# Optimization experiments

Measured on AMD Instinct MI355X. Metric: run time of the kernel, lower is better.

The kernel has to match this reference:

```python
import jax, jax.numpy as jnp
import numpy as np

EMBED = 32; HEADS = 4; HD = 8; FFN = 64; OBS = 64; CTX = 128; BATCH = 16
INIT_SCALE = 1.0 / np.sqrt(2.0 * 5.0)  # 1/sqrt(2*(3 spatial + 2 temporal))


def rmsnorm(x, w, eps=1e-6):
    return x / jnp.sqrt(jnp.mean(x * x, axis=-1, keepdims=True) + eps) * w


def rope_cache(T):
    theta = 1.0 / (10000.0 ** (jnp.arange(0, HD, 2, dtype=jnp.float32) / HD))
    freqs = jnp.arange(T, dtype=jnp.float32)[:, None] * theta[None, :]  # [T, HD//2]
    return jnp.cos(freqs), jnp.sin(freqs)


def apply_rope(x, cos, sin):
    half = x.shape[-1] // 2
    x1, x2 = x[..., :half], x[..., half:]
    c, s = cos[None, None], sin[None, None]  # broadcast over [B, H, T, HD//2]
    return jnp.concatenate([x1 * c - x2 * s, x2 * c + x1 * s], axis=-1)


def attn_block(x, Wq, Wk, Wv, Wo, Wg, Wval, Wout, norm4, qkn, cos=None, sin=None):
    B, S, W = x.shape
    h = rmsnorm(x, norm4[0])

    def proj(Wm):
        return jnp.einsum('bsw,dw->bsd', h, Wm).reshape(B, S, HEADS, HD).transpose(0, 2, 1, 3)

    q = rmsnorm(proj(Wq), qkn[0])
    k = rmsnorm(proj(Wk), qkn[1])
    v = proj(Wv)
    if cos is not None:
        q = apply_rope(q, cos, sin)
        k = apply_rope(k, cos, sin)
    scores = jnp.einsum('bhqd,bhkd->bhqk', q, k) / np.float32(np.sqrt(HD))
    o = jnp.einsum('bhqk,bhkd->bhqd', jax.nn.softmax(scores, axis=-1), v)
    o = o.transpose(0, 2, 1, 3).reshape(B, S, W)
    x = x + rmsnorm(jnp.einsum('bsw,dw->bsd', o, Wo), norm4[1])
    h2 = rmsnorm(x, norm4[2])
    ffn = jax.nn.silu(jnp.einsum('bsw,fw->bsf', h2, Wg)) * jnp.einsum('bsw,fw->bsf', h2, Wval)
    x = x + rmsnorm(jnp.einsum('bsf,wf->bsw', ffn, Wout), norm4[3])
    return x


def setup_inputs():
    key = jax.random.key(0)
    ks = iter(jax.random.split(key, 40))
    sd = 1.0 / np.sqrt(EMBED)
    inp = {
        'obs_seq': jax.random.normal(next(ks), (BATCH, CTX, OBS), jnp.float32),
        'W_val': jax.random.normal(next(ks), (EMBED, 1), jnp.float32),
        'b_val': jnp.zeros((EMBED,), jnp.float32),
        'input_norm_w': jnp.ones((EMBED,), jnp.float32),
        'dim_embed': jax.random.normal(next(ks), (OBS, EMBED), jnp.float32),
        'cls_tokens': jax.random.normal(next(ks), (3, EMBED), jnp.float32) * sd,
        'final_norm_w': jnp.ones((EMBED,), jnp.float32),
    }
    for pre, n in (('s', 3), ('t', 2)):
        inp[pre + '_Wq'] = jax.random.normal(next(ks), (n, EMBED, EMBED), jnp.float32) * sd
        inp[pre + '_Wk'] = jax.random.normal(next(ks), (n, EMBED, EMBED), jnp.float32) * sd
        inp[pre + '_Wv'] = jax.random.normal(next(ks), (n, EMBED, EMBED), jnp.float32) * sd
        inp[pre + '_Wo'] = jax.random.normal(next(ks), (n, EMBED, EMBED), jnp.float32) * (0.1 * INIT_SCALE * sd)
        inp[pre + '_Wg'] = jax.random.normal(next(ks), (n, FFN, EMBED), jnp.float32) * sd
        inp[pre + '_Wval'] = jax.random.normal(next(ks), (n, FFN, EMBED), jnp.float32) * sd
        inp[pre + '_Wout'] = jax.random.normal(next(ks), (n, EMBED, FFN), jnp.float32) * (INIT_SCALE / np.sqrt(FFN))
        inp[pre + '_norm4'] = jnp.ones((n, 4, EMBED), jnp.float32)
        inp[pre + '_qkn'] = jnp.ones((n, 2, HD), jnp.float32)
    return inp


def reference(obs_seq, W_val, b_val, input_norm_w, dim_embed, cls_tokens, final_norm_w,
              s_Wq, s_Wk, s_Wv, s_Wo, s_Wg, s_Wval, s_Wout, s_norm4, s_qkn,
              t_Wq, t_Wk, t_Wv, t_Wo, t_Wg, t_Wval, t_Wout, t_norm4, t_qkn):
    B, T, D = obs_seq.shape
    slots = D + 3
    # value_proj: Linear(1, EMBED) applied to each scalar feature
    tok = obs_seq[..., None] * W_val[:, 0] + b_val            # [B, T, D, EMBED]
    tok = tok + dim_embed[None, None]                          # dim id embedding
    cls = jnp.broadcast_to(cls_tokens[None, None], (B, T, 3, EMBED))
    tokens = rmsnorm(jnp.concatenate([tok, cls], axis=2), input_norm_w)  # [B,T,slots,EMBED]
    cos, sin = rope_cache(T)

    def spatial(tk, i):
        x = tk.reshape(B * T, slots, EMBED)
        x = attn_block(x, s_Wq[i], s_Wk[i], s_Wv[i], s_Wo[i], s_Wg[i], s_Wval[i], s_Wout[i], s_norm4[i], s_qkn[i])
        return x.reshape(B, T, slots, EMBED)

    def temporal(tk, i):
        x = tk.transpose(0, 2, 1, 3).reshape(B * slots, T, EMBED)
        x = attn_block(x, t_Wq[i], t_Wk[i], t_Wv[i], t_Wo[i], t_Wg[i], t_Wval[i], t_Wout[i], t_norm4[i], t_qkn[i], cos, sin)
        return x.reshape(B, slots, T, EMBED).transpose(0, 2, 1, 3)

    tokens = spatial(tokens, 0)
    tokens = temporal(tokens, 0)
    tokens = spatial(tokens, 1)
    tokens = temporal(tokens, 1)
    tokens = spatial(tokens, 2)
    tokens = rmsnorm(tokens, final_norm_w)
    last = tokens[:, -1]  # [B, slots, EMBED]
    return last[:, D], last[:, D + 1], last[:, D + 2]
```

## Files before the change

kernel.cpp:

```cpp
#include <hip/hip_runtime.h>

#define B_ 16
#define T_ 128
#define OBS_ 64
#define SLOTS_ 67
#define E_ 32
#define H_ 4
#define HD_ 8
#define FFN_ 64

typedef _Float16 h2 __attribute__((ext_vector_type(2)));
typedef _Float16 h4 __attribute__((ext_vector_type(4)));
typedef _Float16 h8 __attribute__((ext_vector_type(8)));
typedef __fp16 mh4 __attribute__((ext_vector_type(4)));
typedef __fp16 mh8 __attribute__((ext_vector_type(8)));
typedef float fx4 __attribute__((ext_vector_type(4)));
union H4u { h4 v; h2 h[2]; };

#define WBLK 10240
#define X16_BYTES (B_ * T_ * SLOTS_ * E_ * 2)
#define W16_BYTES (5 * WBLK * 2)
#define ROPE_OFF (X16_BYTES + W16_BYTES)
#define EMBED_BLOCKS (B_ * T_ * SLOTS_ / 64)

__device__ __forceinline__ float red32(float v) {
  v += __shfl_xor(v, 16); v += __shfl_xor(v, 8); v += __shfl_xor(v, 4);
  v += __shfl_xor(v, 2);  v += __shfl_xor(v, 1);
  return v;
}
__device__ __forceinline__ float red8(float v) {
  v += __shfl_xor(v, 4); v += __shfl_xor(v, 2); v += __shfl_xor(v, 1);
  return v;
}
__device__ __forceinline__ float bfly16(float v) {
  v += __shfl_xor(v, 1); v += __shfl_xor(v, 2);
  v += __shfl_xor(v, 4); v += __shfl_xor(v, 8);
  return v;
}
__device__ __forceinline__ h2 pkrtz(float x, float y) {
  return __builtin_bit_cast(h2, __builtin_amdgcn_cvt_pkrtz(x, y));
}
__device__ __forceinline__ float rcp_(float x) { return __builtin_amdgcn_rcpf(x); }
__device__ __forceinline__ float rsq_(float x) { return __builtin_amdgcn_rsqf(x); }
__device__ __forceinline__ fx4 mfma16(h8 a, h8 b, fx4 c) {
  return __builtin_amdgcn_mfma_f32_16x16x32_f16(
      __builtin_bit_cast(mh8, a), __builtin_bit_cast(mh8, b), c, 0, 0, 0);
}
__device__ __forceinline__ fx4 mfma16k16(h4 a, h4 b, fx4 c) {
  return __builtin_amdgcn_mfma_f32_16x16x16f16(
      __builtin_bit_cast(mh4, a), __builtin_bit_cast(mh4, b), c, 0, 0, 0);
}

__device__ __forceinline__ int sw32(int row, int col) {
  return row * 32 + (col ^ (((row >> 1) & 3) << 3));
}
__device__ __forceinline__ int sw64(int row, int col) {
  return row * 64 + (col ^ ((row & 7) << 3));
}

struct WPtrs {
  const float *sWq, *sWk, *sWv, *sWo, *sWg, *sWvl, *sWout;
  const float *tWq, *tWk, *tWv, *tWo, *tWg, *tWvl, *tWout;
};

#define CVT_BLOCKS 100

__global__ __launch_bounds__(256) void setup_kernel(
    WPtrs p, _Float16* __restrict__ dst,
    const float* __restrict__ obs, const float* __restrict__ Wval,
    const float* __restrict__ bval, const float* __restrict__ innw,
    const float* __restrict__ dimemb, const float* __restrict__ cls,
    float2* __restrict__ rope, _Float16* __restrict__ X) {
  if (blockIdx.x < CVT_BLOCKS) {
    int i = blockIdx.x * 256 + threadIdx.x;
    const int total_pairs = 5 * WBLK / 2;
    if (i >= total_pairs) return;
    int blk = i / (WBLK / 2);
    int f = (i % (WBLK / 2)) * 2;
    bool sp = blk < 3;
    int bi = sp ? blk : blk - 3;
    const float* src;
    int o;
    if (f < 1024)      { src = (sp ? p.sWq : p.tWq) + bi * 1024;  o = f; }
    else if (f < 2048) { src = (sp ? p.sWk : p.tWk) + bi * 1024;  o = f - 1024; }
    else if (f < 3072) { src = (sp ? p.sWv : p.tWv) + bi * 1024;  o = f - 2048; }
    else if (f < 4096) { src = (sp ? p.sWo : p.tWo) + bi * 1024;  o = f - 3072; }
    else if (f < 6144) { src = (sp ? p.sWg : p.tWg) + bi * 2048;  o = f - 4096; }
    else if (f < 8192) { src = (sp ? p.sWvl : p.tWvl) + bi * 2048; o = f - 6144; }
    else               { src = (sp ? p.sWout : p.tWout) + bi * 2048; o = f - 8192; }
    ((h2*)dst)[i] = pkrtz(src[o], src[o + 1]);
  } else if (blockIdx.x < CVT_BLOCKS + EMBED_BLOCKS) {
    int t0 = (blockIdx.x - CVT_BLOCKS) * 64 + (threadIdx.x >> 5);
    int e = threadIdx.x & 31;
#pragma unroll
    for (int i = 0; i < 8; i++) {
      int tok = t0 + i * 8;
      int slot = tok % SLOTS_;
      int bt = tok / SLOTS_;
      float v;
      if (slot < OBS_) {
        float o = obs[bt * OBS_ + slot];
        v = o * Wval[e] + bval[e] + dimemb[slot * E_ + e];
      } else {
        v = cls[(slot - OBS_) * E_ + e];
      }
      float ss = red32(v * v);
      X[tok * E_ + e] = (_Float16)(v * rsq_(ss * (1.0f / E_) + 1e-6f) * innw[e]);
    }
  } else {
    for (int i = threadIdx.x; i < T_ * 4; i += 256) {
      int pos = i >> 2, j = i & 3;
      float th = __builtin_amdgcn_exp2f(-(float)j * 3.3219280948873623f);
      float sv, cv;
      __sincosf((float)pos * th, &sv, &cv);
      rope[i] = make_float2(cv, sv);
    }
  }
}

template <int SV, int SP, bool TEMPORAL, bool LAST>
__device__ __forceinline__ void block_body(
    _Float16* __restrict__ X, const _Float16* __restrict__ W16,
    const float* __restrict__ norm4, const float* __restrict__ qkn,
    const float2* __restrict__ rope, const float* __restrict__ fnw,
    float* __restrict__ out, int bid) {
  constexpr int MT = SP / 16;
  constexpr int MTW = (MT + 3) / 4;
  constexpr int VSTRIDE = TEMPORAL ? 128 : 168;
  constexpr int VROWS = TEMPORAL ? 32 : 33;
  __shared__ __align__(16) _Float16 smem[SP * 96 + VROWS * VSTRIDE];
  _Float16* hb = smem;
  _Float16* qb = smem + SP * 32;
  _Float16* kb = smem + SP * 64;
  _Float16* vT = smem + SP * 96;
  _Float16* ffnb = qb;

  const int tid = threadIdx.x;
  const int l = tid & 63, wv = tid >> 6;
  const int lm = l & 15, lq = l >> 4, hd = l & 7;

  auto vt_idx = [](int d, int s) {
    if (TEMPORAL) return d * 128 + (((s & ~15) ^ ((d & 7) << 4)) | (s & 15));
    return d * VSTRIDE + s;
  };

  int base, stride;
  if (TEMPORAL) {
    int b = bid / SLOTS_;
    int slot = bid % SLOTS_;
    base = (b * T_ * SLOTS_ + slot) * E_;
    stride = SLOTS_ * E_;
  } else {
    base = bid * 2 * SLOTS_ * E_;
    stride = E_;
  }

  const float nw0a = norm4[lm],      nw0b = norm4[16 + lm];
  const float nw1a = norm4[32 + lm], nw1b = norm4[48 + lm];
  const float nw2a = norm4[64 + lm], nw2b = norm4[80 + lm];
  const float nw3a = norm4[96 + lm], nw3b = norm4[112 + lm];
  const fx4 fz = {0.f, 0.f, 0.f, 0.f};
  const float qw = qkn[hd], kw = qkn[8 + hd];
  const float qscale = 0.35355339059327373f * 1.4426950408889634f;

  float xr[MTW][4][2];
#pragma unroll
  for (int t = 0; t < MTW; t++) {
    int mt = wv + 4 * t;
    if (mt < MT) {
#pragma unroll
      for (int r = 0; r < 4; r++) {
        int s = mt * 16 + lq * 4 + r;
        bool ok = (SV == SP) || (s < SV);
        int off = base + s * stride;
        xr[t][r][0] = ok ? (float)X[off + lm] : 0.f;
        xr[t][r][1] = ok ? (float)X[off + 16 + lm] : 0.f;
      }
    }
  }
#pragma unroll
  for (int t = 0; t < MTW; t++) {
    int mt = wv + 4 * t;
    if (mt < MT) {
#pragma unroll
      for (int r = 0; r < 4; r++) {
        int s = mt * 16 + lq * 4 + r;
        float p = bfly16(xr[t][r][0] * xr[t][r][0] + xr[t][r][1] * xr[t][r][1]);
        float inv = rsq_(p * (1.0f / E_) + 1e-6f);
        if (SV == SP || s < SV) {
          hb[sw32(s, lm)] = (_Float16)(xr[t][r][0] * inv * nw0a);
          hb[sw32(s, 16 + lm)] = (_Float16)(xr[t][r][1] * inv * nw0b);
        }
      }
    }
  }
  __syncthreads();

  for (int u = wv; u < MT * 2; u += 4) {
    const int mt = u >> 1, nt = u & 1;
    h8 aH = *(const h8*)(hb + sw32(mt * 16 + lm, lq * 8));
    float rc[4], rs[4];
    if (TEMPORAL) {
#pragma unroll
      for (int r = 0; r < 4; r++) {
        float2 cs = rope[(mt * 16 + lq * 4 + r) * 4 + (hd & 3)];
        rc[r] = cs.x; rs[r] = cs.y;
      }
    }
    const int d = nt * 16 + lm;
    h8 bq = *(const h8*)(W16 + (nt * 16 + lm) * 32 + lq * 8);
    h8 bk = *(const h8*)(W16 + 1024 + (nt * 16 + lm) * 32 + lq * 8);
    h8 bv = *(const h8*)(W16 + 2048 + (nt * 16 + lm) * 32 + lq * 8);
    fx4 aq = mfma16(aH, bq, fz);
    fx4 ak = mfma16(aH, bk, fz);
    fx4 av = mfma16(aH, bv, fz);
#pragma unroll
    for (int r = 0; r < 4; r++) {
      int s = mt * 16 + lq * 4 + r;
      float q1 = aq[r], k1 = ak[r];
      float qv = q1 * rsq_(red8(q1 * q1) * 0.125f + 1e-6f) * qw;
      float kv = k1 * rsq_(red8(k1 * k1) * 0.125f + 1e-6f) * kw;
      if (TEMPORAL) {
        float qp = __shfl_xor(qv, 4);
        float kp = __shfl_xor(kv, 4);
        qv = (hd < 4) ? (qv * rc[r] - qp * rs[r]) : (qv * rc[r] + qp * rs[r]);
        kv = (hd < 4) ? (kv * rc[r] - kp * rs[r]) : (kv * rc[r] + kp * rs[r]);
      }
      if (SV == SP || s < SV) {
        qb[sw32(s, d)] = (_Float16)(qv * qscale);
        kb[sw32(s, d)] = (_Float16)kv;
      }
    }
    const int s0 = mt * 16 + lq * 4;
    const int va = vt_idx(d, s0);
    if (SV == SP || s0 + 1 < SV) *(h2*)(vT + va) = pkrtz(av[0], av[1]);
    if (SV == SP || s0 + 3 < SV) *(h2*)(vT + va + 2) = pkrtz(av[2], av[3]);
  }
  if (!TEMPORAL) {
    for (int idx = tid; idx < 32 * 13; idx += 256) {
      int d = idx / 13, c = 2 * SLOTS_ + 2 * (idx % 13);
      *(h2*)(vT + d * VSTRIDE + c) = pkrtz(0.f, 0.f);
    }
    for (int idx = tid; idx < VSTRIDE / 2; idx += 256) {
      *(h2*)(vT + 32 * VSTRIDE + 2 * idx) = pkrtz(1.f, 1.f);
    }
  }
  __syncthreads();

  {
    const int h = wv;
    const h8 z8 = {};
    const h4 ones4 = {(_Float16)1.f, (_Float16)1.f, (_Float16)1.f, (_Float16)1.f};
    const bool vlane = (lm < 8);
    const int dv = h * 8 + (lm & 7);
    const int vrow = (!TEMPORAL && !vlane) ? 32 : dv;

    auto loadQ = [&](int mt) {
      h8 b = *(const h8*)(qb + sw32(mt * 16 + lm, lq * 8));
      return (lq == h) ? b : z8;
    };
    auto maskx = [&](float x, int kidx, int mode, int q) {
      if (mode == 1) return (kidx < SLOTS_) ? x : 0.f;
      if (mode == 2) return (kidx >= SLOTS_) ? x : 0.f;
      if (mode == 3) return (kidx < 2 * SLOTS_) ? x : 0.f;
      if (mode == 4) {
        bool ok = (kidx < 2 * SLOTS_) && ((kidx < SLOTS_) == (q < SLOTS_));
        return ok ? x : 0.f;
      }
      return x;
    };
    auto ktile2 = [&](int kt, int mode, const h8& bQ0, const h8& bQ1,
                      fx4& o0, fx4& o1) {
      h8 aK = *(const h8*)(kb + sw32(kt * 16 + lm, lq * 8));
      fx4 s0 = mfma16(aK, bQ0, fz);
      fx4 s1 = mfma16(aK, bQ1, fz);
      float e0[4], e1[4];
#pragma unroll
      for (int r = 0; r < 4; r++) {
        int kidx = kt * 16 + lq * 4 + r;
        e0[r] = maskx(__builtin_amdgcn_exp2f(s0[r]), kidx, mode, 0);
        e1[r] = maskx(__builtin_amdgcn_exp2f(s1[r]), kidx, mode, 0);
      }
      H4u p0, p1;
      p0.h[0] = pkrtz(e0[0], e0[1]); p0.h[1] = pkrtz(e0[2], e0[3]);
      p1.h[0] = pkrtz(e1[0], e1[1]); p1.h[1] = pkrtz(e1[2], e1[3]);
      h4 aV = *(const h4*)(vT + vt_idx(vrow, kt * 16 + lq * 4));
      if (TEMPORAL) aV = vlane ? aV : ones4;
      o0 = mfma16k16(aV, p0.v, o0);
      o1 = mfma16k16(aV, p1.v, o1);
    };
    auto ktile1 = [&](int kt, int mode, int q, const h8& bQ, fx4& oa) {
      h8 aK = *(const h8*)(kb + sw32(kt * 16 + lm, lq * 8));
      fx4 sc = mfma16(aK, bQ, fz);
      float ev[4];
#pragma unroll
      for (int r = 0; r < 4; r++) {
        int kidx = kt * 16 + lq * 4 + r;
        ev[r] = maskx(__builtin_amdgcn_exp2f(sc[r]), kidx, mode, q);
      }
      H4u pT;
      pT.h[0] = pkrtz(ev[0], ev[1]); pT.h[1] = pkrtz(ev[2], ev[3]);
      h4 aV = *(const h4*)(vT + vt_idx(vrow, kt * 16 + lq * 4));
      if (TEMPORAL) aV = vlane ? aV : ones4;
      oa = mfma16k16(aV, pT.v, oa);
    };
    auto finish = [&](int mt, fx4& oa) {
      int q = mt * 16 + lm;
      float lsum = __shfl_xor(oa[0], 32);
      float inv = rcp_(lsum);
      if (lq < 2 && (SV == SP || q < SV)) {
        H4u ov;
        ov.h[0] = pkrtz(oa[0] * inv, oa[1] * inv);
        ov.h[1] = pkrtz(oa[2] * inv, oa[3] * inv);
        *(h4*)(hb + sw32(q, h * 8 + lq * 4)) = ov.v;
      }
    };

    if (TEMPORAL) {
      for (int mtp = 0; mtp < MT / 2; mtp++) {
        h8 bQ0 = loadQ(2 * mtp), bQ1 = loadQ(2 * mtp + 1);
        fx4 o0 = fz, o1 = fz;
#pragma unroll
        for (int kt = 0; kt < MT; kt++) ktile2(kt, 0, bQ0, bQ1, o0, o1);
        finish(2 * mtp, o0);
        finish(2 * mtp + 1, o1);
      }
    } else {
      for (int mtp = 0; mtp < 2; mtp++) {
        h8 bQ0 = loadQ(2 * mtp), bQ1 = loadQ(2 * mtp + 1);
        fx4 o0 = fz, o1 = fz;
#pragma unroll
        for (int kt = 0; kt < 4; kt++) ktile2(kt, 0, bQ0, bQ1, o0, o1);
        ktile2(4, 1, bQ0, bQ1, o0, o1);
        finish(2 * mtp, o0);
        finish(2 * mtp + 1, o1);
      }
      {
        h8 bQ = loadQ(4);
        fx4 oa = fz;
        const int q = 4 * 16 + lm;
#pragma unroll
        for (int kt = 0; kt < MT; kt++) ktile1(kt, 4, q, bQ, oa);
        finish(4, oa);
      }
      for (int mtp = 0; mtp < 2; mtp++) {
        int m0 = 5 + 2 * mtp;
        h8 bQ0 = loadQ(m0), bQ1 = loadQ(m0 + 1);
        fx4 o0 = fz, o1 = fz;
        ktile2(4, 2, bQ0, bQ1, o0, o1);
#pragma unroll
        for (int kt = 5; kt < 8; kt++) ktile2(kt, 0, bQ0, bQ1, o0, o1);
        ktile2(8, 3, bQ0, bQ1, o0, o1);
        finish(m0, o0);
        finish(m0 + 1, o1);
      }
    }
  }
  __syncthreads();

#pragma unroll
  for (int t = 0; t < MTW; t++) {
    int mt = wv + 4 * t;
    if (mt < MT) {
      h8 aO = *(const h8*)(hb + sw32(mt * 16 + lm, lq * 8));
      h8 b0 = *(const h8*)(W16 + 3072 + lm * 32 + lq * 8);
      h8 b1 = *(const h8*)(W16 + 3072 + (16 + lm) * 32 + lq * 8);
      fx4 a0 = mfma16(aO, b0, fz);
      fx4 a1 = mfma16(aO, b1, fz);
#pragma unroll
      for (int r = 0; r < 4; r++) {
        int s = mt * 16 + lq * 4 + r;
        float p = bfly16(a0[r] * a0[r] + a1[r] * a1[r]);
        float inv = rsq_(p * (1.0f / E_) + 1e-6f);
        xr[t][r][0] += a0[r] * inv * nw1a;
        xr[t][r][1] += a1[r] * inv * nw1b;
        float q2 = bfly16(xr[t][r][0] * xr[t][r][0] + xr[t][r][1] * xr[t][r][1]);
        float inv2 = rsq_(q2 * (1.0f / E_) + 1e-6f);
        if (SV == SP || s < SV) {
          hb[sw32(s, lm)] = (_Float16)(xr[t][r][0] * inv2 * nw2a);
          hb[sw32(s, 16 + lm)] = (_Float16)(xr[t][r][1] * inv2 * nw2b);
        }
      }
    }
  }
  __syncthreads();

  for (int u = wv; u < MT * 4; u += 4) {
    const int mt = u >> 2, nt = u & 3;
    h8 aH2 = *(const h8*)(hb + sw32(mt * 16 + lm, lq * 8));
    h8 bg = *(const h8*)(W16 + 4096 + (nt * 16 + lm) * 32 + lq * 8);
    h8 bl = *(const h8*)(W16 + 6144 + (nt * 16 + lm) * 32 + lq * 8);
    fx4 g = mfma16(aH2, bg, fz);
    fx4 vvv = mfma16(aH2, bl, fz);
#pragma unroll
    for (int r = 0; r < 4; r++) {
      int s = mt * 16 + lq * 4 + r;
      if (SV == SP || s < SV) {
        float gg = g[r];
        float sg = gg * rcp_(1.0f + __builtin_amdgcn_exp2f(gg * -1.4426950408889634f));
        ffnb[sw64(s, nt * 16 + lm)] = (_Float16)(sg * vvv[r]);
      }
    }
  }
  __syncthreads();

#pragma unroll
  for (int t = 0; t < MTW; t++) {
    int mt = wv + 4 * t;
    if (mt < MT) {
      const int row = mt * 16 + lm;
      h8 a0 = *(const h8*)(ffnb + sw64(row, lq * 8));
      h8 a1 = *(const h8*)(ffnb + sw64(row, 32 + lq * 8));
      h8 b00 = *(const h8*)(W16 + 8192 + lm * 64 + lq * 8);
      h8 b01 = *(const h8*)(W16 + 8192 + lm * 64 + 32 + lq * 8);
      h8 b10 = *(const h8*)(W16 + 8192 + (16 + lm) * 64 + lq * 8);
      h8 b11 = *(const h8*)(W16 + 8192 + (16 + lm) * 64 + 32 + lq * 8);
      fx4 o0 = mfma16(a1, b01, mfma16(a0, b00, fz));
      fx4 o1 = mfma16(a1, b11, mfma16(a0, b10, fz));
#pragma unroll
      for (int r = 0; r < 4; r++) {
        int s = mt * 16 + lq * 4 + r;
        float p = bfly16(o0[r] * o0[r] + o1[r] * o1[r]);
        float inv = rsq_(p * (1.0f / E_) + 1e-6f);
        xr[t][r][0] += o0[r] * inv * nw3a;
        xr[t][r][1] += o1[r] * inv * nw3b;
        if (SV == SP || s < SV) {
          int off = base + s * stride;
          X[off + lm] = (_Float16)xr[t][r][0];
          X[off + 16 + lm] = (_Float16)xr[t][r][1];
        }
      }
      if (LAST && mt == MT - 1 && (bid & (T_ / 2 - 1)) == (T_ / 2 - 1)) {
        const int b = bid / (T_ / 2);
#pragma unroll
        for (int r = 0; r < 4; r++) {
          int s = mt * 16 + lq * 4 + r;
          int j = s - (SLOTS_ + OBS_);
          float p2 = bfly16(xr[t][r][0] * xr[t][r][0] + xr[t][r][1] * xr[t][r][1]);
          if (j >= 0 && j < 3) {
            float inv2 = rsq_(p2 * (1.0f / E_) + 1e-6f);
            out[j * (B_ * E_) + b * E_ + lm] = xr[t][r][0] * inv2 * fnw[lm];
            out[j * (B_ * E_) + b * E_ + 16 + lm] = xr[t][r][1] * inv2 * fnw[16 + lm];
          }
        }
      }
    }
  }
}

__global__ __launch_bounds__(256, 4) void attn_spatial_kernel(
    _Float16* __restrict__ X, const _Float16* __restrict__ W16,
    const float* __restrict__ norm4, const float* __restrict__ qkn) {
  block_body<2 * SLOTS_, 144, false, false>(X, W16, norm4, qkn, nullptr,
                                            nullptr, nullptr, blockIdx.x);
}

__global__ __launch_bounds__(256, 4) void attn_spatial_last_kernel(
    _Float16* __restrict__ X, const _Float16* __restrict__ W16,
    const float* __restrict__ norm4, const float* __restrict__ qkn,
    const float* __restrict__ fnw, float* __restrict__ out) {
  block_body<2 * SLOTS_, 144, false, true>(X, W16, norm4, qkn, nullptr,
                                           fnw, out, blockIdx.x);
}

__global__ __launch_bounds__(256, 5) void attn_temporal_kernel(
    _Float16* __restrict__ X, const _Float16* __restrict__ W16,
    const float* __restrict__ norm4, const float* __restrict__ qkn,
    const float2* __restrict__ rope) {
  block_body<T_, 128, true, false>(X, W16, norm4, qkn, rope,
                                   nullptr, nullptr, blockIdx.x);
}

extern "C" void kernel_launch(void* const* d_in, const int* in_sizes, int n_in,
                              void* d_out, int out_size, void* d_ws, size_t ws_size,
                              hipStream_t stream) {
  (void)in_sizes; (void)n_in; (void)out_size; (void)ws_size;
  const float* obs          = (const float*)d_in[0];
  const float* W_val        = (const float*)d_in[1];
  const float* b_val        = (const float*)d_in[2];
  const float* input_norm_w = (const float*)d_in[3];
  const float* dim_embed    = (const float*)d_in[4];
  const float* cls_tokens   = (const float*)d_in[5];
  const float* final_norm_w = (const float*)d_in[6];
  const float* s_n4   = (const float*)d_in[14];
  const float* s_qkn  = (const float*)d_in[15];
  const float* t_n4   = (const float*)d_in[23];
  const float* t_qkn  = (const float*)d_in[24];

  _Float16* X = (_Float16*)d_ws;
  _Float16* W16 = (_Float16*)((char*)d_ws + X16_BYTES);
  float2* rope = (float2*)((char*)d_ws + ROPE_OFF);
  float* out = (float*)d_out;

  WPtrs wp;
  wp.sWq   = (const float*)d_in[7];
  wp.sWk   = (const float*)d_in[8];
  wp.sWv   = (const float*)d_in[9];
  wp.sWo   = (const float*)d_in[10];
  wp.sWg   = (const float*)d_in[11];
  wp.sWvl  = (const float*)d_in[12];
  wp.sWout = (const float*)d_in[13];
  wp.tWq   = (const float*)d_in[16];
  wp.tWk   = (const float*)d_in[17];
  wp.tWv   = (const float*)d_in[18];
  wp.tWo   = (const float*)d_in[19];
  wp.tWg   = (const float*)d_in[20];
  wp.tWvl  = (const float*)d_in[21];
  wp.tWout = (const float*)d_in[22];

  setup_kernel<<<CVT_BLOCKS + EMBED_BLOCKS + 1, 256, 0, stream>>>(
      wp, W16, obs, W_val, b_val, input_norm_w, dim_embed, cls_tokens, rope, X);

  const int N4 = 4 * E_;
  const int QN = 2 * HD_;

#define SPATIAL(i)                                                     \
  attn_spatial_kernel<<<B_ * T_ / 2, 256, 0, stream>>>(                \
      X, W16 + (i)*WBLK, s_n4 + (i)*N4, s_qkn + (i)*QN)
#define TEMPORAL(i)                                                    \
  attn_temporal_kernel<<<B_ * SLOTS_, 256, 0, stream>>>(               \
      X, W16 + (3 + (i)) * WBLK, t_n4 + (i)*N4, t_qkn + (i)*QN, rope)

  SPATIAL(0);
  TEMPORAL(0);
  SPATIAL(1);
  TEMPORAL(1);
  attn_spatial_last_kernel<<<B_ * T_ / 2, 256, 0, stream>>>(
      X, W16 + 2 * WBLK, s_n4 + 2 * N4, s_qkn + 2 * QN, final_norm_w, out);

#undef SPATIAL
#undef TEMPORAL
}
```

Before: 312.3 us.

## Hoist weights and K/V/Q fragments into registers, prefetch LDS tiles in projections

Each wave now loads its fixed weight columns once for the QKV, output, gate and down projections, and prefetches the next activation tile from LDS while computing the current one. The attention stage preloads all K, V and Q fragments into register arrays before looping, and the temporal path now processes four query tiles per key pass instead of two. The embed kernel drops to one token per warp with more blocks. These changes cut repeated LDS and global loads and expose more independent MFMA work, at the cost of more register pressure, which may reduce occupancy under launch_bounds(256,4).

```diff
diff --git a/kernel.cpp b/kernel.cpp
--- a/kernel.cpp
+++ b/kernel.cpp
@@ -21,7 +21,7 @@
 #define X16_BYTES (B_ * T_ * SLOTS_ * E_ * 2)
 #define W16_BYTES (5 * WBLK * 2)
 #define ROPE_OFF (X16_BYTES + W16_BYTES)
-#define EMBED_BLOCKS (B_ * T_ * SLOTS_ / 64)
+#define EMBED_BLOCKS ((B_ * T_ * SLOTS_ + 7) / 8)
 
 __device__ __forceinline__ float red32(float v) {
   v += __shfl_xor(v, 16); v += __shfl_xor(v, 8); v += __shfl_xor(v, 4);
@@ -90,23 +90,21 @@
     else               { src = (sp ? p.sWout : p.tWout) + bi * 2048; o = f - 8192; }
     ((h2*)dst)[i] = pkrtz(src[o], src[o + 1]);
   } else if (blockIdx.x < CVT_BLOCKS + EMBED_BLOCKS) {
-    int t0 = (blockIdx.x - CVT_BLOCKS) * 64 + (threadIdx.x >> 5);
+    int tok = (blockIdx.x - CVT_BLOCKS) * 8 + (threadIdx.x >> 5);
     int e = threadIdx.x & 31;
-#pragma unroll
-    for (int i = 0; i < 8; i++) {
-      int tok = t0 + i * 8;
-      int slot = tok % SLOTS_;
-      int bt = tok / SLOTS_;
-      float v;
-      if (slot < OBS_) {
-        float o = obs[bt * OBS_ + slot];
-        v = o * Wval[e] + bval[e] + dimemb[slot * E_ + e];
-      } else {
-        v = cls[(slot - OBS_) * E_ + e];
-      }
-      float ss = red32(v * v);
-      X[tok * E_ + e] = (_Float16)(v * rsq_(ss * (1.0f / E_) + 1e-6f) * innw[e]);
-    }
+    const int total = B_ * T_ * SLOTS_;
+    if (tok >= total) return;
+    int slot = tok % SLOTS_;
+    int bt = tok / SLOTS_;
+    float v;
+    if (slot < OBS_) {
+      float o = obs[bt * OBS_ + slot];
+      v = o * Wval[e] + bval[e] + dimemb[slot * E_ + e];
+    } else {
+      v = cls[(slot - OBS_) * E_ + e];
+    }
+    float ss = red32(v * v);
+    X[tok * E_ + e] = (_Float16)(v * rsq_(ss * (1.0f / E_) + 1e-6f) * innw[e]);
   } else {
     for (int i = threadIdx.x; i < T_ * 4; i += 256) {
       int pos = i >> 2, j = i & 3;
@@ -196,45 +194,53 @@
   }
   __syncthreads();
 
-  for (int u = wv; u < MT * 2; u += 4) {
-    const int mt = u >> 1, nt = u & 1;
-    h8 aH = *(const h8*)(hb + sw32(mt * 16 + lm, lq * 8));
-    float rc[4], rs[4];
-    if (TEMPORAL) {
+  {
+    const int ntw = wv & 1;
+    const int d = ntw * 16 + lm;
+    h8 bqw = *(const h8*)(W16 + (ntw * 16 + lm) * 32 + lq * 8);
+    h8 bkw = *(const h8*)(W16 + 1024 + (ntw * 16 + lm) * 32 + lq * 8);
+    h8 bvw = *(const h8*)(W16 + 2048 + (ntw * 16 + lm) * 32 + lq * 8);
+    int u = wv;
+    h8 aH = *(const h8*)(hb + sw32((u >> 1) * 16 + lm, lq * 8));
+    for (; u < MT * 2; u += 4) {
+      h8 aHn;
+      if (u + 4 < MT * 2)
+        aHn = *(const h8*)(hb + sw32(((u + 4) >> 1) * 16 + lm, lq * 8));
+      const int mt = u >> 1;
+      float rc[4], rs[4];
+      if (TEMPORAL) {
+#pragma unroll
+        for (int r = 0; r < 4; r++) {
+          float2 cs = rope[(mt * 16 + lq * 4 + r) * 4 + (hd & 3)];
+          rc[r] = cs.x; rs[r] = cs.y;
+        }
+      }
+      fx4 aq = mfma16(aH, bqw, fz);
+      fx4 ak = mfma16(aH, bkw, fz);
+      fx4 av = mfma16(aH, bvw, fz);
 #pragma unroll
       for (int r = 0; r < 4; r++) {
-        float2 cs = rope[(mt * 16 + lq * 4 + r) * 4 + (hd & 3)];
-        rc[r] = cs.x; rs[r] = cs.y;
-      }
-    }
-    const int d = nt * 16 + lm;
-    h8 bq = *(const h8*)(W16 + (nt * 16 + lm) * 32 + lq * 8);
-    h8 bk = *(const h8*)(W16 + 1024 + (nt * 16 + lm) * 32 + lq * 8);
-    h8 bv = *(const h8*)(W16 + 2048 + (nt * 16 + lm) * 32 + lq * 8);
-    fx4 aq = mfma16(aH, bq, fz);
-    fx4 ak = mfma16(aH, bk, fz);
-    fx4 av = mfma16(aH, bv, fz);
-#pragma unroll
-    for (int r = 0; r < 4; r++) {
-      int s = mt * 16 + lq * 4 + r;
-      float q1 = aq[r], k1 = ak[r];
-      float qv = q1 * rsq_(red8(q1 * q1) * 0.125f + 1e-6f) * qw;
-      float kv = k1 * rsq_(red8(k1 * k1) * 0.125f + 1e-6f) * kw;
-      if (TEMPORAL) {
-        float qp = __shfl_xor(qv, 4);
-        float kp = __shfl_xor(kv, 4);
-        qv = (hd < 4) ? (qv * rc[r] - qp * rs[r]) : (qv * rc[r] + qp * rs[r]);
-        kv = (hd < 4) ? (kv * rc[r] - kp * rs[r]) : (kv * rc[r] + kp * rs[r]);
-      }
-      if (SV == SP || s < SV) {
-        qb[sw32(s, d)] = (_Float16)(qv * qscale);
-        kb[sw32(s, d)] = (_Float16)kv;
-      }
-    }
-    const int s0 = mt * 16 + lq * 4;
-    const int va = vt_idx(d, s0);
-    if (SV == SP || s0 + 1 < SV) *(h2*)(vT + va) = pkrtz(av[0], av[1]);
-    if (SV == SP || s0 + 3 < SV) *(h2*)(vT + va + 2) = pkrtz(av[2], av[3]);
+        int s = mt * 16 + lq * 4 + r;
+        float q1 = aq[r], k1 = ak[r];
+        float qv = q1 * rsq_(red8(q1 * q1) * 0.125f + 1e-6f) * qw;
+        float kv = k1 * rsq_(red8(k1 * k1) * 0.125f + 1e-6f) * kw;
+        if (TEMPORAL) {
+          float qp = __shfl_xor(qv, 4);
+          float kp = __shfl_xor(kv, 4);
+          qv = (hd < 4) ? (qv * rc[r] - qp * rs[r]) : (qv * rc[r] + qp * rs[r]);
+          kv = (hd < 4) ? (kv * rc[r] - kp * rs[r]) : (kv * rc[r] + kp * rs[r]);
+        }
+        if (SV == SP || s < SV) {
+          qb[sw32(s, d)] = (_Float16)(qv * qscale);
+          kb[sw32(s, d)] = (_Float16)kv;
+        }
+      }
+      const int s0 = mt * 16 + lq * 4;
+      const int va = vt_idx(d, s0);
+      if (SV == SP || s0 + 1 < SV) *(h2*)(vT + va) = pkrtz(av[0], av[1]);
+      if (SV == SP || s0 + 3 < SV) *(h2*)(vT + va + 2) = pkrtz(av[2], av[3]);
+      aH = aHn;
+    }
   }
   if (!TEMPORAL) {
     for (int idx = tid; idx < 32 * 13; idx += 256) {
@@ -255,10 +261,16 @@
     const int dv = h * 8 + (lm & 7);
     const int vrow = (!TEMPORAL && !vlane) ? 32 : dv;
 
-    auto loadQ = [&](int mt) {
-      h8 b = *(const h8*)(qb + sw32(mt * 16 + lm, lq * 8));
-      return (lq == h) ? b : z8;
-    };
+    h8 aK[MT]; h4 aV[MT]; h8 bQ[MT];
+#pragma unroll
+    for (int kt = 0; kt < MT; kt++) {
+      aK[kt] = *(const h8*)(kb + sw32(kt * 16 + lm, lq * 8));
+      h4 v = *(const h4*)(vT + vt_idx(vrow, kt * 16 + lq * 4));
+      aV[kt] = (TEMPORAL && !vlane) ? ones4 : v;
+      h8 qf = *(const h8*)(qb + sw32(kt * 16 + lm, lq * 8));
+      bQ[kt] = (lq == h) ? qf : z8;
+    }
+
     auto maskx = [&](float x, int kidx, int mode, int q) {
       if (mode == 1) return (kidx < SLOTS_) ? x : 0.f;
       if (mode == 2) return (kidx >= SLOTS_) ? x : 0.f;
@@ -269,29 +281,7 @@
       }
       return x;
     };
-    auto ktile2 = [&](int kt, int mode, const h8& bQ0, const h8& bQ1,
-                      fx4& o0, fx4& o1) {
-      h8 aK = *(const h8*)(kb + sw32(kt * 16 + lm, lq * 8));
-      fx4 s0 = mfma16(aK, bQ0, fz);
-      fx4 s1 = mfma16(aK, bQ1, fz);
-      float e0[4], e1[4];
-#pragma unroll
-      for (int r = 0; r < 4; r++) {
-        int kidx = kt * 16 + lq * 4 + r;
-        e0[r] = maskx(__builtin_amdgcn_exp2f(s0[r]), kidx, mode, 0);
-        e1[r] = maskx(__builtin_amdgcn_exp2f(s1[r]), kidx, mode, 0);
-      }
-      H4u p0, p1;
-      p0.h[0] = pkrtz(e0[0], e0[1]); p0.h[1] = pkrtz(e0[2], e0[3]);
-      p1.h[0] = pkrtz(e1[0], e1[1]); p1.h[1] = pkrtz(e1[2], e1[3]);
-      h4 aV = *(const h4*)(vT + vt_idx(vrow, kt * 16 + lq * 4));
-      if (TEMPORAL) aV = vlane ? aV : ones4;
-      o0 = mfma16k16(aV, p0.v, o0);
-      o1 = mfma16k16(aV, p1.v, o1);
-    };
-    auto ktile1 = [&](int kt, int mode, int q, const h8& bQ, fx4& oa) {
-      h8 aK = *(const h8*)(kb + sw32(kt * 16 + lm, lq * 8));
-      fx4 sc = mfma16(aK, bQ, fz);
+    auto pvstep = [&](int kt, int mode, int q, const fx4& sc, fx4& oacc) {
       float ev[4];
 #pragma unroll
       for (int r = 0; r < 4; r++) {
@@ -300,9 +290,7 @@
       }
       H4u pT;
       pT.h[0] = pkrtz(ev[0], ev[1]); pT.h[1] = pkrtz(ev[2], ev[3]);
-      h4 aV = *(const h4*)(vT + vt_idx(vrow, kt * 16 + lq * 4));
-      if (TEMPORAL) aV = vlane ? aV : ones4;
-      oa = mfma16k16(aV, pT.v, oa);
+      oacc = mfma16k16(aV[kt], pT.v, oacc);
     };
     auto finish = [&](int mt, fx4& oa) {
       int q = mt * 16 + lm;
@@ -317,40 +305,58 @@
     };
 
     if (TEMPORAL) {
-      for (int mtp = 0; mtp < MT / 2; mtp++) {
-        h8 bQ0 = loadQ(2 * mtp), bQ1 = loadQ(2 * mtp + 1);
+#pragma unroll
+      for (int half = 0; half < 2; half++) {
+        fx4 o[4] = {fz, fz, fz, fz};
+#pragma unroll
+        for (int kt = 0; kt < MT; kt++) {
+          fx4 s0 = mfma16(aK[kt], bQ[half * 4 + 0], fz);
+          fx4 s1 = mfma16(aK[kt], bQ[half * 4 + 1], fz);
+          fx4 s2 = mfma16(aK[kt], bQ[half * 4 + 2], fz);
+          fx4 s3 = mfma16(aK[kt], bQ[half * 4 + 3], fz);
+          pvstep(kt, 0, 0, s0, o[0]);
+          pvstep(kt, 0, 0, s1, o[1]);
+          pvstep(kt, 0, 0, s2, o[2]);
+          pvstep(kt, 0, 0, s3, o[3]);
+        }
+#pragma unroll
+        for (int j = 0; j < 4; j++) finish(half * 4 + j, o[j]);
+      }
+    } else {
+      auto kpair = [&](int kt, int mode, int m0, fx4& o0, fx4& o1) {
+        fx4 s0 = mfma16(aK[kt], bQ[m0], fz);
+        fx4 s1 = mfma16(aK[kt], bQ[m0 + 1], fz);
+        pvstep(kt, mode, 0, s0, o0);
+        pvstep(kt, mode, 0, s1, o1);
+      };
+#pragma unroll
+      for (int mtp = 0; mtp < 2; mtp++) {
+        int m0 = 2 * mtp;
         fx4 o0 = fz, o1 = fz;
 #pragma unroll
-        for (int kt = 0; kt < MT; kt++) ktile2(kt, 0, bQ0, bQ1, o0, o1);
-        finish(2 * mtp, o0);
-        finish(2 * mtp + 1, o1);
-      }
-    } else {
-      for (int mtp = 0; mtp < 2; mtp++) {
-        h8 bQ0 = loadQ(2 * mtp), bQ1 = loadQ(2 * mtp + 1);
-        fx4 o0 = fz, o1 = fz;
-#pragma unroll
-        for (int kt = 0; kt < 4; kt++) ktile2(kt, 0, bQ0, bQ1, o0, o1);
-        ktile2(4, 1, bQ0, bQ1, o0, o1);
-        finish(2 * mtp, o0);
-        finish(2 * mtp + 1, o1);
+        for (int kt = 0; kt < 4; kt++) kpair(kt, 0, m0, o0, o1);
+        kpair(4, 1, m0, o0, o1);
+        finish(m0, o0);
+        finish(m0 + 1, o1);
       }
       {
-        h8 bQ = loadQ(4);
         fx4 oa = fz;
         const int q = 4 * 16 + lm;
 #pragma unroll
-        for (int kt = 0; kt < MT; kt++) ktile1(kt, 4, q, bQ, oa);
+        for (int kt = 0; kt < MT; kt++) {
+          fx4 sc = mfma16(aK[kt], bQ[4], fz);
+          pvstep(kt, 4, q, sc, oa);
+        }
         finish(4, oa);
       }
+#pragma unroll
       for (int mtp = 0; mtp < 2; mtp++) {
         int m0 = 5 + 2 * mtp;
-        h8 bQ0 = loadQ(m0), bQ1 = loadQ(m0 + 1);
         fx4 o0 = fz, o1 = fz;
-        ktile2(4, 2, bQ0, bQ1, o0, o1);
-#pragma unroll
-        for (int kt = 5; kt < 8; kt++) ktile2(kt, 0, bQ0, bQ1, o0, o1);
-        ktile2(8, 3, bQ0, bQ1, o0, o1);
+        kpair(4, 2, m0, o0, o1);
+#pragma unroll
+        for (int kt = 5; kt < 8; kt++) kpair(kt, 0, m0, o0, o1);
+        kpair(8, 3, m0, o0, o1);
         finish(m0, o0);
         finish(m0 + 1, o1);
       }
@@ -358,89 +364,113 @@
   }
   __syncthreads();
 
-#pragma unroll
-  for (int t = 0; t < MTW; t++) {
-    int mt = wv + 4 * t;
-    if (mt < MT) {
-      h8 aO = *(const h8*)(hb + sw32(mt * 16 + lm, lq * 8));
-      h8 b0 = *(const h8*)(W16 + 3072 + lm * 32 + lq * 8);
-      h8 b1 = *(const h8*)(W16 + 3072 + (16 + lm) * 32 + lq * 8);
-      fx4 a0 = mfma16(aO, b0, fz);
-      fx4 a1 = mfma16(aO, b1, fz);
+  {
+    h8 b0w = *(const h8*)(W16 + 3072 + lm * 32 + lq * 8);
+    h8 b1w = *(const h8*)(W16 + 3072 + (16 + lm) * 32 + lq * 8);
+    h8 aO[MTW];
+#pragma unroll
+    for (int t = 0; t < MTW; t++) {
+      int mt = wv + 4 * t;
+      if (mt < MT) aO[t] = *(const h8*)(hb + sw32(mt * 16 + lm, lq * 8));
+    }
+#pragma unroll
+    for (int t = 0; t < MTW; t++) {
+      int mt = wv + 4 * t;
+      if (mt < MT) {
+        fx4 a0 = mfma16(aO[t], b0w, fz);
+        fx4 a1 = mfma16(aO[t], b1w, fz);
+#pragma unroll
+        for (int r = 0; r < 4; r++) {
+          int s = mt * 16 + lq * 4 + r;
+          float p = bfly16(a0[r] * a0[r] + a1[r] * a1[r]);
+          float inv = rsq_(p * (1.0f / E_) + 1e-6f);
+          xr[t][r][0] += a0[r] * inv * nw1a;
+          xr[t][r][1] += a1[r] * inv * nw1b;
+          float q2 = bfly16(xr[t][r][0] * xr[t][r][0] + xr[t][r][1] * xr[t][r][1]);
+          float inv2 = rsq_(q2 * (1.0f / E_) + 1e-6f);
+          if (SV == SP || s < SV) {
+            hb[sw32(s, lm)] = (_Float16)(xr[t][r][0] * inv2 * nw2a);
+            hb[sw32(s, 16 + lm)] = (_Float16)(xr[t][r][1] * inv2 * nw2b);
+          }
+        }
+      }
+    }
+  }
+  __syncthreads();
+
+  {
+    const int ntw = wv;
+    h8 bg = *(const h8*)(W16 + 4096 + (ntw * 16 + lm) * 32 + lq * 8);
+    h8 bl = *(const h8*)(W16 + 6144 + (ntw * 16 + lm) * 32 + lq * 8);
+    int u = wv;
+    h8 aH2 = *(const h8*)(hb + sw32((u >> 2) * 16 + lm, lq * 8));
+    for (; u < MT * 4; u += 4) {
+      h8 nxt;
+      if (u + 4 < MT * 4)
+        nxt = *(const h8*)(hb + sw32(((u + 4) >> 2) * 16 + lm, lq * 8));
+      const int mt = u >> 2;
+      fx4 g = mfma16(aH2, bg, fz);
+      fx4 vvv = mfma16(aH2, bl, fz);
 #pragma unroll
       for (int r = 0; r < 4; r++) {
         int s = mt * 16 + lq * 4 + r;
-        float p = bfly16(a0[r] * a0[r] + a1[r] * a1[r]);
-        float inv = rsq_(p * (1.0f / E_) + 1e-6f);
-        xr[t][r][0] += a0[r] * inv * nw1a;
-        xr[t][r][1] += a1[r] * inv * nw1b;
-        float q2 = bfly16(xr[t][r][0] * xr[t][r][0] + xr[t][r][1] * xr[t][r][1]);
-        float inv2 = rsq_(q2 * (1.0f / E_) + 1e-6f);
         if (SV == SP || s < SV) {
-          hb[sw32(s, lm)] = (_Float16)(xr[t][r][0] * inv2 * nw2a);
-          hb[sw32(s, 16 + lm)] = (_Float16)(xr[t][r][1] * inv2 * nw2b);
-        }
-      }
+          float gg = g[r];
+          float sg = gg * rcp_(1.0f + __builtin_amdgcn_exp2f(gg * -1.4426950408889634f));
+          ffnb[sw64(s, ntw * 16 + lm)] = (_Float16)(sg * vvv[r]);
+        }
+      }
+      aH2 = nxt;
     }
   }
   __syncthreads();
 
-  for (int u = wv; u < MT * 4; u += 4) {
-    const int mt = u >> 2, nt = u & 3;
-    h8 aH2 = *(const h8*)(hb + sw32(mt * 16 + lm, lq * 8));
-    h8 bg = *(const h8*)(W16 + 4096 + (nt * 16 + lm) * 32 + lq * 8);
-    h8 bl = *(const h8*)(W16 + 6144 + (nt * 16 + lm) * 32 + lq * 8);
-    fx4 g = mfma16(aH2, bg, fz);
-    fx4 vvv = mfma16(aH2, bl, fz);
-#pragma unroll
-    for (int r = 0; r < 4; r++) {
-      int s = mt * 16 + lq * 4 + r;
-      if (SV == SP || s < SV) {
-        float gg = g[r];
-        float sg = gg * rcp_(1.0f + __builtin_amdgcn_exp2f(gg * -1.4426950408889634f));
-        ffnb[sw64(s, nt * 16 + lm)] = (_Float16)(sg * vvv[r]);
-      }
-    }
-  }
-  __syncthreads();
-
-#pragma unroll
-  for (int t = 0; t < MTW; t++) {
-    int mt = wv + 4 * t;
-    if (mt < MT) {
-      const int row = mt * 16 + lm;
-      h8 a0 = *(const h8*)(ffnb + sw64(row, lq * 8));
-      h8 a1 = *(const h8*)(ffnb + sw64(row, 32 + lq * 8));
-      h8 b00 = *(const h8*)(W16 + 8192 + lm * 64 + lq * 8);
-      h8 b01 = *(const h8*)(W16 + 8192 + lm * 64 + 32 + lq * 8);
-      h8 b10 = *(const h8*)(W16 + 8192 + (16 + lm) * 64 + lq * 8);
-      h8 b11 = *(const h8*)(W16 + 8192 + (16 + lm) * 64 + 32 + lq * 8);
-      fx4 o0 = mfma16(a1, b01, mfma16(a0, b00, fz));
-      fx4 o1 = mfma16(a1, b11, mfma16(a0, b10, fz));
-#pragma unroll
-      for (int r = 0; r < 4; r++) {
-        int s = mt * 16 + lq * 4 + r;
-        float p = bfly16(o0[r] * o0[r] + o1[r] * o1[r]);
-        float inv = rsq_(p * (1.0f / E_) + 1e-6f);
-        xr[t][r][0] += o0[r] * inv * nw3a;
-        xr[t][r][1] += o1[r] * inv * nw3b;
-        if (SV == SP || s < SV) {
-          int off = base + s * stride;
-          X[off + lm] = (_Float16)xr[t][r][0];
-          X[off + 16 + lm] = (_Float16)xr[t][r][1];
-        }
-      }
-      if (LAST && mt == MT - 1 && (bid & (T_ / 2 - 1)) == (T_ / 2 - 1)) {
-        const int b = bid / (T_ / 2);
+  {
+    h8 b00 = *(const h8*)(W16 + 8192 + lm * 64 + lq * 8);
+    h8 b01 = *(const h8*)(W16 + 8192 + lm * 64 + 32 + lq * 8);
+    h8 b10 = *(const h8*)(W16 + 8192 + (16 + lm) * 64 + lq * 8);
+    h8 b11 = *(const h8*)(W16 + 8192 + (16 + lm) * 64 + 32 + lq * 8);
+    h8 f0[MTW], f1[MTW];
+#pragma unroll
+    for (int t = 0; t < MTW; t++) {
+      int mt = wv + 4 * t;
+      if (mt < MT) {
+        const int row = mt * 16 + lm;
+        f0[t] = *(const h8*)(ffnb + sw64(row, lq * 8));
+        f1[t] = *(const h8*)(ffnb + sw64(row, 32 + lq * 8));
+      }
+    }
+#pragma unroll
+    for (int t = 0; t < MTW; t++) {
+      int mt = wv + 4 * t;
+      if (mt < MT) {
+        fx4 o0 = mfma16(f1[t], b01, mfma16(f0[t], b00, fz));
+        fx4 o1 = mfma16(f1[t], b11, mfma16(f0[t], b10, fz));
 #pragma unroll
         for (int r = 0; r < 4; r++) {
           int s = mt * 16 + lq * 4 + r;
-          int j = s - (SLOTS_ + OBS_);
-          float p2 = bfly16(xr[t][r][0] * xr[t][r][0] + xr[t][r][1] * xr[t][r][1]);
-          if (j >= 0 && j < 3) {
-            float inv2 = rsq_(p2 * (1.0f / E_) + 1e-6f);
-            out[j * (B_ * E_) + b * E_ + lm] = xr[t][r][0] * inv2 * fnw[lm];
-            out[j * (B_ * E_) + b * E_ + 16 + lm] = xr[t][r][1] * inv2 * fnw[16 + lm];
+          float p = bfly16(o0[r] * o0[r] + o1[r] * o1[r]);
+          float inv = rsq_(p * (1.0f / E_) + 1e-6f);
+          xr[t][r][0] += o0[r] * inv * nw3a;
+          xr[t][r][1] += o1[r] * inv * nw3b;
+          if (SV == SP || s < SV) {
+            int off = base + s * stride;
+            X[off + lm] = (_Float16)xr[t][r][0];
+            X[off + 16 + lm] = (_Float16)xr[t][r][1];
+          }
+        }
+        if (LAST && mt == MT - 1 && (bid & (T_ / 2 - 1)) == (T_ / 2 - 1)) {
+          const int b = bid / (T_ / 2);
+#pragma unroll
+          for (int r = 0; r < 4; r++) {
+            int s = mt * 16 + lq * 4 + r;
+            int j = s - (SLOTS_ + OBS_);
+            float p2 = bfly16(xr[t][r][0] * xr[t][r][0] + xr[t][r][1] * xr[t][r][1]);
+            if (j >= 0 && j < 3) {
+              float inv2 = rsq_(p2 * (1.0f / E_) + 1e-6f);
+              out[j * (B_ * E_) + b * E_ + lm] = xr[t][r][0] * inv2 * fnw[lm];
+              out[j * (B_ * E_) + b * E_ + 16 + lm] = xr[t][r][1] * inv2 * fnw[16 + lm];
+            }
           }
         }
       }
```

New measurement: 349.2 us. 11.8% more time.

## Hoist K/V fragments into registers across query tiles and split embed blocks

Applied to the files above, without the earlier changes.

In the attention loops, the K and V fragments for all key tiles are loaded once into register arrays and reused across query-tile pairs, where before they were reloaded from LDS for every pair. The temporal kernel's occupancy hint drops from 5 to 4 blocks per CU to leave room for the extra registers. The embedding stage now handles one token per warp-group per block instead of an 8-iteration loop, which launches more, smaller blocks and adds a tail bounds check. The trade is higher register pressure and lower occupancy in exchange for less LDS traffic.

```diff
diff --git a/kernel.cpp b/kernel.cpp
--- a/kernel.cpp
+++ b/kernel.cpp
@@ -21,7 +21,7 @@
 #define X16_BYTES (B_ * T_ * SLOTS_ * E_ * 2)
 #define W16_BYTES (5 * WBLK * 2)
 #define ROPE_OFF (X16_BYTES + W16_BYTES)
-#define EMBED_BLOCKS (B_ * T_ * SLOTS_ / 64)
+#define EMBED_BLOCKS ((B_ * T_ * SLOTS_ + 7) / 8)
 
 __device__ __forceinline__ float red32(float v) {
   v += __shfl_xor(v, 16); v += __shfl_xor(v, 8); v += __shfl_xor(v, 4);
@@ -90,23 +90,21 @@
     else               { src = (sp ? p.sWout : p.tWout) + bi * 2048; o = f - 8192; }
     ((h2*)dst)[i] = pkrtz(src[o], src[o + 1]);
   } else if (blockIdx.x < CVT_BLOCKS + EMBED_BLOCKS) {
-    int t0 = (blockIdx.x - CVT_BLOCKS) * 64 + (threadIdx.x >> 5);
+    int tok = (blockIdx.x - CVT_BLOCKS) * 8 + (threadIdx.x >> 5);
     int e = threadIdx.x & 31;
-#pragma unroll
-    for (int i = 0; i < 8; i++) {
-      int tok = t0 + i * 8;
-      int slot = tok % SLOTS_;
-      int bt = tok / SLOTS_;
-      float v;
-      if (slot < OBS_) {
-        float o = obs[bt * OBS_ + slot];
-        v = o * Wval[e] + bval[e] + dimemb[slot * E_ + e];
-      } else {
-        v = cls[(slot - OBS_) * E_ + e];
-      }
-      float ss = red32(v * v);
-      X[tok * E_ + e] = (_Float16)(v * rsq_(ss * (1.0f / E_) + 1e-6f) * innw[e]);
-    }
+    const int total = B_ * T_ * SLOTS_;
+    if (tok >= total) return;
+    int slot = tok % SLOTS_;
+    int bt = tok / SLOTS_;
+    float v;
+    if (slot < OBS_) {
+      float o = obs[bt * OBS_ + slot];
+      v = o * Wval[e] + bval[e] + dimemb[slot * E_ + e];
+    } else {
+      v = cls[(slot - OBS_) * E_ + e];
+    }
+    float ss = red32(v * v);
+    X[tok * E_ + e] = (_Float16)(v * rsq_(ss * (1.0f / E_) + 1e-6f) * innw[e]);
   } else {
     for (int i = threadIdx.x; i < T_ * 4; i += 256) {
       int pos = i >> 2, j = i & 3;
@@ -255,6 +253,13 @@
     const int dv = h * 8 + (lm & 7);
     const int vrow = (!TEMPORAL && !vlane) ? 32 : dv;
 
+    auto loadK = [&](int kt) {
+      return *(const h8*)(kb + sw32(kt * 16 + lm, lq * 8));
+    };
+    auto loadV = [&](int kt) {
+      h4 v = *(const h4*)(vT + vt_idx(vrow, kt * 16 + lq * 4));
+      return (TEMPORAL && !vlane) ? ones4 : v;
+    };
     auto loadQ = [&](int mt) {
       h8 b = *(const h8*)(qb + sw32(mt * 16 + lm, lq * 8));
       return (lq == h) ? b : z8;
@@ -269,29 +274,8 @@
       }
       return x;
     };
-    auto ktile2 = [&](int kt, int mode, const h8& bQ0, const h8& bQ1,
-                      fx4& o0, fx4& o1) {
-      h8 aK = *(const h8*)(kb + sw32(kt * 16 + lm, lq * 8));
-      fx4 s0 = mfma16(aK, bQ0, fz);
-      fx4 s1 = mfma16(aK, bQ1, fz);
-      float e0[4], e1[4];
-#pragma unroll
-      for (int r = 0; r < 4; r++) {
-        int kidx = kt * 16 + lq * 4 + r;
-        e0[r] = maskx(__builtin_amdgcn_exp2f(s0[r]), kidx, mode, 0);
-        e1[r] = maskx(__builtin_amdgcn_exp2f(s1[r]), kidx, mode, 0);
-      }
-      H4u p0, p1;
-      p0.h[0] = pkrtz(e0[0], e0[1]); p0.h[1] = pkrtz(e0[2], e0[3]);
-      p1.h[0] = pkrtz(e1[0], e1[1]); p1.h[1] = pkrtz(e1[2], e1[3]);
-      h4 aV = *(const h4*)(vT + vt_idx(vrow, kt * 16 + lq * 4));
-      if (TEMPORAL) aV = vlane ? aV : ones4;
-      o0 = mfma16k16(aV, p0.v, o0);
-      o1 = mfma16k16(aV, p1.v, o1);
-    };
-    auto ktile1 = [&](int kt, int mode, int q, const h8& bQ, fx4& oa) {
-      h8 aK = *(const h8*)(kb + sw32(kt * 16 + lm, lq * 8));
-      fx4 sc = mfma16(aK, bQ, fz);
+    auto pvstep = [&](const h4& av, int kt, int mode, int q, const fx4& sc,
+                      fx4& oacc) {
       float ev[4];
 #pragma unroll
       for (int r = 0; r < 4; r++) {
@@ -300,9 +284,7 @@
       }
       H4u pT;
       pT.h[0] = pkrtz(ev[0], ev[1]); pT.h[1] = pkrtz(ev[2], ev[3]);
-      h4 aV = *(const h4*)(vT + vt_idx(vrow, kt * 16 + lq * 4));
-      if (TEMPORAL) aV = vlane ? aV : ones4;
-      oa = mfma16k16(aV, pT.v, oa);
+      oacc = mfma16k16(av, pT.v, oacc);
     };
     auto finish = [&](int mt, fx4& oa) {
       int q = mt * 16 + lm;
@@ -317,42 +299,80 @@
     };
 
     if (TEMPORAL) {
+      h8 aK[MT]; h4 aV[MT];
+#pragma unroll
+      for (int kt = 0; kt < MT; kt++) { aK[kt] = loadK(kt); aV[kt] = loadV(kt); }
+#pragma unroll
       for (int mtp = 0; mtp < MT / 2; mtp++) {
         h8 bQ0 = loadQ(2 * mtp), bQ1 = loadQ(2 * mtp + 1);
         fx4 o0 = fz, o1 = fz;
 #pragma unroll
-        for (int kt = 0; kt < MT; kt++) ktile2(kt, 0, bQ0, bQ1, o0, o1);
+        for (int kt = 0; kt < MT; kt++) {
+          fx4 s0 = mfma16(aK[kt], bQ0, fz);
+          fx4 s1 = mfma16(aK[kt], bQ1, fz);
+          pvstep(aV[kt], kt, 0, 0, s0, o0);
+          pvstep(aV[kt], kt, 0, 0, s1, o1);
+        }
         finish(2 * mtp, o0);
         finish(2 * mtp + 1, o1);
       }
     } else {
-      for (int mtp = 0; mtp < 2; mtp++) {
-        h8 bQ0 = loadQ(2 * mtp), bQ1 = loadQ(2 * mtp + 1);
-        fx4 o0 = fz, o1 = fz;
-#pragma unroll
-        for (int kt = 0; kt < 4; kt++) ktile2(kt, 0, bQ0, bQ1, o0, o1);
-        ktile2(4, 1, bQ0, bQ1, o0, o1);
-        finish(2 * mtp, o0);
-        finish(2 * mtp + 1, o1);
-      }
       {
+        h8 aKw[5]; h4 aVw[5];
+#pragma unroll
+        for (int kt = 0; kt < 5; kt++) { aKw[kt] = loadK(kt); aVw[kt] = loadV(kt); }
+#pragma unroll
+        for (int mtp = 0; mtp < 2; mtp++) {
+          h8 bQ0 = loadQ(2 * mtp), bQ1 = loadQ(2 * mtp + 1);
+          fx4 o0 = fz, o1 = fz;
+#pragma unroll
+          for (int kt = 0; kt < 5; kt++) {
+            int mode = (kt == 4) ? 1 : 0;
+            fx4 s0 = mfma16(aKw[kt], bQ0, fz);
+            fx4 s1 = mfma16(aKw[kt], bQ1, fz);
+            pvstep(aVw[kt], kt, mode, 0, s0, o0);
+            pvstep(aVw[kt], kt, mode, 0, s1, o1);
+          }
+          finish(2 * mtp, o0);
+          finish(2 * mtp + 1, o1);
+        }
+      }
+      {
+        h8 aKw[9]; h4 aVw[9];
+#pragma unroll
+        for (int kt = 0; kt < 9; kt++) { aKw[kt] = loadK(kt); aVw[kt] = loadV(kt); }
         h8 bQ = loadQ(4);
         fx4 oa = fz;
         const int q = 4 * 16 + lm;
 #pragma unroll
-        for (int kt = 0; kt < MT; kt++) ktile1(kt, 4, q, bQ, oa);
+        for (int kt = 0; kt < 9; kt++) {
+          fx4 sc = mfma16(aKw[kt], bQ, fz);
+          pvstep(aVw[kt], kt, 4, q, sc, oa);
+        }
         finish(4, oa);
       }
-      for (int mtp = 0; mtp < 2; mtp++) {
-        int m0 = 5 + 2 * mtp;
-        h8 bQ0 = loadQ(m0), bQ1 = loadQ(m0 + 1);
-        fx4 o0 = fz, o1 = fz;
-        ktile2(4, 2, bQ0, bQ1, o0, o1);
-#pragma unroll
-        for (int kt = 5; kt < 8; kt++) ktile2(kt, 0, bQ0, bQ1, o0, o1);
-        ktile2(8, 3, bQ0, bQ1, o0, o1);
-        finish(m0, o0);
-        finish(m0 + 1, o1);
+      {
+        h8 aKw[5]; h4 aVw[5];
+#pragma unroll
+        for (int kt = 0; kt < 5; kt++) {
+          aKw[kt] = loadK(kt + 4); aVw[kt] = loadV(kt + 4);
+        }
+#pragma unroll
+        for (int mtp = 0; mtp < 2; mtp++) {
+          int m0 = 5 + 2 * mtp;
+          h8 bQ0 = loadQ(m0), bQ1 = loadQ(m0 + 1);
+          fx4 o0 = fz, o1 = fz;
+#pragma unroll
+          for (int kt = 0; kt < 5; kt++) {
+            int mode = (kt == 0) ? 2 : (kt == 4 ? 3 : 0);
+            fx4 s0 = mfma16(aKw[kt], bQ0, fz);
+            fx4 s1 = mfma16(aKw[kt], bQ1, fz);
+            pvstep(aVw[kt], kt + 4, mode, 0, s0, o0);
+            pvstep(aVw[kt], kt + 4, mode, 0, s1, o1);
+          }
+          finish(m0, o0);
+          finish(m0 + 1, o1);
+        }
       }
     }
   }
@@ -463,7 +483,7 @@
                                            fnw, out, blockIdx.x);
 }
 
-__global__ __launch_bounds__(256, 5) void attn_temporal_kernel(
+__global__ __launch_bounds__(256, 4) void attn_temporal_kernel(
     _Float16* __restrict__ X, const _Float16* __restrict__ W16,
     const float* __restrict__ norm4, const float* __restrict__ qkn,
     const float2* __restrict__ rope) {
```

Result: faster. 305.1 us (-2.3%).
